# Optimization experiments

Measured on AMD Instinct MI355X. Metric: run time of the kernel, lower is better.

Reference implementation:

```python
import jax, jax.numpy as jnp
import numpy as np

EMBED_DIM = 256
NUM_HEADS = 8
PROJ_DIM = EMBED_DIM // NUM_HEADS


def setup_inputs() -> dict:
    key = jax.random.key(0)
    ks = jax.random.split(key, 5)
    scale = 1.0 / np.sqrt(EMBED_DIM)
    inputs = jax.random.normal(ks[0], (2, 12, 12, 12, EMBED_DIM), dtype=jnp.float32)
    Wq = jax.random.normal(ks[1], (EMBED_DIM, EMBED_DIM), dtype=jnp.float32) * scale
    Wk = jax.random.normal(ks[2], (EMBED_DIM, EMBED_DIM), dtype=jnp.float32) * scale
    Wv = jax.random.normal(ks[3], (EMBED_DIM, EMBED_DIM), dtype=jnp.float32) * scale
    Wo = jax.random.normal(ks[4], (EMBED_DIM, EMBED_DIM), dtype=jnp.float32) * scale
    z = jnp.zeros((EMBED_DIM,), dtype=jnp.float32)
    return {"inputs": inputs, "Wq": Wq, "bq": z, "Wk": Wk, "bk": z,
            "Wv": Wv, "bv": z, "Wo": Wo, "bo": z}


def reference(inputs, Wq, bq, Wk, bk, Wv, bv, Wo, bo):
    B, h, w, d, E = inputs.shape
    S = h * w * d  # flattened spatial sequence
    x = inputs.reshape(B, S, E)
    # projections + head split: [B, S, E] -> [B, H, S, P]
    def split_heads(t):
        return t.reshape(B, S, NUM_HEADS, PROJ_DIM).transpose(0, 2, 1, 3)
    q = split_heads(x @ Wq + bq)
    k = split_heads(x @ Wk + bk)
    v = split_heads(x @ Wv + bv)
    # NOTE: original module does NOT scale by 1/sqrt(proj_dim)
    scores = jnp.einsum('bhsp,bhtp->bhst', q, k)  # [B, H, S, S]
    attn = jax.nn.softmax(scores, axis=-1)
    out = jnp.einsum('bhst,bhtp->bhsp', attn, v)  # [B, H, S, P]
    out = out.transpose(0, 2, 1, 3).reshape(B, h, w, d, E)
    return out @ Wo + bo
```

## Files before the change

### kernel.cpp

```cpp
#include <hip/hip_runtime.h>
#include <math.h>

#define EMBED 256
#define HEADS 8
#define PDIM  32
#define BATCH 2
#define SEQ   1728
#define NTOK  (BATCH*SEQ)
#define NE    (NTOK*EMBED)
#define NKT   (SEQ/64)
#define NPAIR ((NKT+1)/2)
#define WSZ   (EMBED*EMBED)
#define XCH   (NE/8)
#define WCH   (WSZ/8)
#define LOG2E 1.44269504088896f

typedef __attribute__((ext_vector_type(8))) __bf16 bf16x8;
typedef __attribute__((ext_vector_type(4))) float  f32x4;
typedef unsigned short ushort_t;
typedef unsigned int   uint_t;

static __device__ __forceinline__ unsigned short f2bf_rne(float f) {
    union { float f; unsigned u; } x; x.f = f;
    unsigned r = x.u + 0x7fffu + ((x.u >> 16) & 1u);
    return (unsigned short)(r >> 16);
}
union v8cast { uint4 u; bf16x8 v; };

static __device__ __forceinline__ void cvt8_hilo(const float f[8], bf16x8& hi, bf16x8& lo) {
    uint4 ph, pl;
    uint_t* phv = (uint_t*)&ph; uint_t* plv = (uint_t*)&pl;
    #pragma unroll
    for (int j = 0; j < 4; ++j) {
        const float f0 = f[2 * j], f1 = f[2 * j + 1];
        const uint_t u0 = __float_as_uint(f0) + 0x8000u;
        const uint_t u1 = __float_as_uint(f1) + 0x8000u;
        phv[j] = __builtin_amdgcn_perm(u1, u0, 0x07060302u);
        const float l0 = f0 - __uint_as_float(u0 & 0xFFFF0000u);
        const float l1 = f1 - __uint_as_float(u1 & 0xFFFF0000u);
        plv[j] = __builtin_amdgcn_perm(__float_as_uint(l1) + 0x8000u,
                                       __float_as_uint(l0) + 0x8000u, 0x07060302u);
    }
    v8cast ch; ch.u = ph; hi = ch.v;
    v8cast cl; cl.u = pl; lo = cl.v;
}

__global__ __launch_bounds__(256) void prep_kernel(
    const float* __restrict__ x,
    const float* __restrict__ Wq, const float* __restrict__ Wk,
    const float* __restrict__ Wv, const float* __restrict__ Wo,
    ushort_t* __restrict__ xhi, ushort_t* __restrict__ xlo,
    ushort_t* __restrict__ wthi, ushort_t* __restrict__ wtlo,
    ushort_t* __restrict__ wot)
{
    const int id = blockIdx.x * 256 + threadIdx.x;
    if (id < XCH) {
        float f[8];
        *(float4*)&f[0] = *(const float4*)(x + (size_t)id * 8);
        *(float4*)&f[4] = *(const float4*)(x + (size_t)id * 8 + 4);
        bf16x8 hi, lo; cvt8_hilo(f, hi, lo);
        v8cast ch; ch.v = hi; *(uint4*)&xhi[(size_t)id * 8] = ch.u;
        v8cast cl; cl.v = lo; *(uint4*)&xlo[(size_t)id * 8] = cl.u;
    } else if (id < XCH + 3 * WCH) {
        int r = id - XCH;
        const int z = r / WCH; r -= z * WCH;
        const float* __restrict__ W = (z == 0) ? Wq : (z == 1) ? Wk : Wv;
        const int n = r >> 5, kc = (r & 31) * 8;
        float f[8];
        #pragma unroll
        for (int j = 0; j < 8; ++j) f[j] = W[(size_t)(kc + j) * EMBED + n];
        bf16x8 hi, lo; cvt8_hilo(f, hi, lo);
        v8cast ch; ch.v = hi; *(uint4*)&wthi[(size_t)z * WSZ + n * EMBED + kc] = ch.u;
        v8cast cl; cl.v = lo; *(uint4*)&wtlo[(size_t)z * WSZ + n * EMBED + kc] = cl.u;
    } else {
        int r = id - XCH - 3 * WCH;
        const int n = r >> 5, kc = (r & 31) * 8;
        float f[8];
        #pragma unroll
        for (int j = 0; j < 8; ++j) f[j] = Wo[(size_t)(kc + j) * EMBED + n];
        bf16x8 hi, lo; cvt8_hilo(f, hi, lo);
        v8cast ch; ch.v = hi; *(uint4*)&wot[n * EMBED + kc] = ch.u;
    }
}

__global__ __launch_bounds__(64) void qkv_gemm_kernel(
    const ushort_t* __restrict__ xhi, const ushort_t* __restrict__ xlo,
    const ushort_t* __restrict__ wthi, const ushort_t* __restrict__ wtlo,
    const float* __restrict__ bq, const float* __restrict__ bk, const float* __restrict__ bv,
    ushort_t* __restrict__ qo, ushort_t* __restrict__ ko, ushort_t* __restrict__ vt)
{
    const int lane = threadIdx.x, li = lane & 15, quad = lane >> 4;
    const int m0 = blockIdx.x * 32, n0 = blockIdx.y * 32, z = blockIdx.z;
    const float* __restrict__ bias = (z == 0) ? bq : (z == 1) ? bk : bv;

    const ushort_t* ahp = xhi + (size_t)(m0 + li) * EMBED + quad * 8;
    const ushort_t* alp = xlo + (size_t)(m0 + li) * EMBED + quad * 8;
    const ushort_t* bhp = wthi + (size_t)z * WSZ + (size_t)(n0 + li) * EMBED + quad * 8;
    const ushort_t* blp = wtlo + (size_t)z * WSZ + (size_t)(n0 + li) * EMBED + quad * 8;

    f32x4 acc[2][2];
    #pragma unroll
    for (int mt = 0; mt < 2; ++mt)
        #pragma unroll
        for (int nt = 0; nt < 2; ++nt)
            acc[mt][nt] = (f32x4){0.f, 0.f, 0.f, 0.f};

    #pragma unroll 2
    for (int k0 = 0; k0 < EMBED; k0 += 32) {
        bf16x8 ah[2], al[2], bh[2], bl[2];
        #pragma unroll
        for (int mt = 0; mt < 2; ++mt) {
            ah[mt] = *(const bf16x8*)(ahp + (size_t)mt * 16 * EMBED + k0);
            al[mt] = *(const bf16x8*)(alp + (size_t)mt * 16 * EMBED + k0);
        }
        #pragma unroll
        for (int nt = 0; nt < 2; ++nt) {
            bh[nt] = *(const bf16x8*)(bhp + (size_t)nt * 16 * EMBED + k0);
            bl[nt] = *(const bf16x8*)(blp + (size_t)nt * 16 * EMBED + k0);
        }
        #pragma unroll
        for (int mt = 0; mt < 2; ++mt)
            #pragma unroll
            for (int nt = 0; nt < 2; ++nt) {
                acc[mt][nt] = __builtin_amdgcn_mfma_f32_16x16x32_bf16(ah[mt], bh[nt], acc[mt][nt], 0, 0, 0);
                acc[mt][nt] = __builtin_amdgcn_mfma_f32_16x16x32_bf16(al[mt], bh[nt], acc[mt][nt], 0, 0, 0);
                acc[mt][nt] = __builtin_amdgcn_mfma_f32_16x16x32_bf16(ah[mt], bl[nt], acc[mt][nt], 0, 0, 0);
            }
    }

    const int b = m0 / SEQ;
    const int sbase = m0 - b * SEQ;

    if (z <= 1) {
        ushort_t* __restrict__ dst = z ? ko : qo;
        #pragma unroll
        for (int nt = 0; nt < 2; ++nt) {
            const int gcol = n0 + nt * 16 + li;
            const int h = gcol >> 5, p = gcol & 31;
            const float bb = bias[gcol];
            ushort_t* base = dst + ((size_t)(b * HEADS + h) * SEQ) * PDIM + p;
            #pragma unroll
            for (int mt = 0; mt < 2; ++mt)
                #pragma unroll
                for (int r = 0; r < 4; ++r) {
                    const int s = sbase + mt * 16 + quad * 4 + r;
                    base[(size_t)s * PDIM] = f2bf_rne(acc[mt][nt][r] + bb);
                }
        }
    } else {
        #pragma unroll
        for (int nt = 0; nt < 2; ++nt) {
            const int gcol = n0 + nt * 16 + li;
            const int h = gcol >> 5, p = gcol & 31;
            const float bb = bias[gcol];
            ushort_t* base = vt + ((size_t)(b * HEADS + h) * PDIM + p) * SEQ;
            #pragma unroll
            for (int mt = 0; mt < 2; ++mt) {
                const int s0 = sbase + mt * 16 + quad * 4;
                ushort4 w;
                w.x = f2bf_rne(acc[mt][nt][0] + bb);
                w.y = f2bf_rne(acc[mt][nt][1] + bb);
                w.z = f2bf_rne(acc[mt][nt][2] + bb);
                w.w = f2bf_rne(acc[mt][nt][3] + bb);
                *(ushort4*)&base[s0] = w;
            }
        }
    }
}

__global__ __launch_bounds__(512, 4) void attn_kernel(
    const ushort_t* __restrict__ q, const ushort_t* __restrict__ k,
    const ushort_t* __restrict__ vt, ushort_t* __restrict__ aob)
{
    const int t    = threadIdx.x;
    const int lane = t & 63;
    const int w    = t >> 6;
    const int li   = lane & 15;
    const int quad = lane >> 4;
    const int qg   = w >> 1, half = w & 1;
    const int bh = blockIdx.y;
    const int b  = bh >> 3, h = bh & 7;
    const int q0 = blockIdx.x * 64 + qg * 16;

    const ushort_t* __restrict__ qb = q  + (size_t)bh * SEQ * PDIM;
    const ushort_t* __restrict__ kb = k  + (size_t)bh * SEQ * PDIM;
    const ushort_t* __restrict__ vb = vt + (size_t)bh * PDIM * SEQ;

    __shared__ ushort_t Ks[2][2][64][40];
    __shared__ ushort_t Vs[2][2][32][72];
    __shared__ ushort_t Ps[8][16][72];
    __shared__ float    Om[8][16][33];
    __shared__ float    Ml[8][2][16];

    const bf16x8 qfrag = *(const bf16x8*)(qb + (size_t)(q0 + li) * PDIM + quad * 8);

    const int ktil = t >> 8;
    const int krow = (t >> 2) & 63, kck = (t & 3) * 8;
    const int vrow = (t >> 3) & 31, vcv = (t & 7) * 8;
    const ushort_t* kgp = kb + (size_t)(ktil * 64 + krow) * PDIM + kck;
    const ushort_t* vgp = vb + (size_t)vrow * SEQ + ktil * 64 + vcv;

    f32x4 o0 = {0.f, 0.f, 0.f, 0.f};
    f32x4 o1 = {0.f, 0.f, 0.f, 0.f};
    float m_run = -__builtin_inff(), l_run = 0.f;

    uint4 kreg = *(const uint4*)(kgp);
    uint4 vreg = *(const uint4*)(vgp);

    #pragma unroll 2
    for (int i = 0; i < NPAIR; ++i) {
        const int p = i & 1;
        *(uint4*)&Ks[p][ktil][krow][kck] = kreg;
        *(uint4*)&Vs[p][ktil][vrow][vcv] = vreg;
        __syncthreads();
        if (i + 1 < NPAIR && 2 * (i + 1) + ktil < NKT) {
            kreg = *(const uint4*)(kgp + (size_t)(2 * (i + 1)) * 64 * PDIM);
            vreg = *(const uint4*)(vgp + 2 * (i + 1) * 64);
        }
        const int kt = 2 * i + half;
        if (kt < NKT) {
            const f32x4 zero = {0.f, 0.f, 0.f, 0.f};
            f32x4 st[4];
            #pragma unroll
            for (int jt = 0; jt < 4; ++jt) {
                const bf16x8 kf = *(const bf16x8*)&Ks[p][half][jt * 16 + li][quad * 8];
                st[jt] = __builtin_amdgcn_mfma_f32_16x16x32_bf16(kf, qfrag, zero, 0, 0, 0);
            }

            float tm = fmaxf(fmaxf(fmaxf(st[0][0], st[0][1]), fmaxf(st[0][2], st[0][3])),
                             fmaxf(fmaxf(st[1][0], st[1][1]), fmaxf(st[1][2], st[1][3])));
            tm = fmaxf(tm, fmaxf(fmaxf(fmaxf(st[2][0], st[2][1]), fmaxf(st[2][2], st[2][3])),
                                 fmaxf(fmaxf(st[3][0], st[3][1]), fmaxf(st[3][2], st[3][3]))));
            tm = fmaxf(tm, __shfl_xor(tm, 16));
            tm = fmaxf(tm, __shfl_xor(tm, 32));
            const float mnew  = fmaxf(m_run, tm);
            const float negml = -(mnew * LOG2E);

            float ps = 0.f;
            #pragma unroll
            for (int jt = 0; jt < 4; ++jt) {
                const float p0 = __builtin_amdgcn_exp2f(fmaf(st[jt][0], LOG2E, negml));
                const float p1 = __builtin_amdgcn_exp2f(fmaf(st[jt][1], LOG2E, negml));
                const float p2 = __builtin_amdgcn_exp2f(fmaf(st[jt][2], LOG2E, negml));
                const float p3 = __builtin_amdgcn_exp2f(fmaf(st[jt][3], LOG2E, negml));
                ps += (p0 + p1) + (p2 + p3);
                uint2 pw;
                pw.x = __builtin_amdgcn_perm(__float_as_uint(p1) + 0x8000u,
                                             __float_as_uint(p0) + 0x8000u, 0x07060302u);
                pw.y = __builtin_amdgcn_perm(__float_as_uint(p3) + 0x8000u,
                                             __float_as_uint(p2) + 0x8000u, 0x07060302u);
                *(uint2*)&Ps[w][li][16 * jt + 4 * quad] = pw;
            }
            ps += __shfl_xor(ps, 16);
            ps += __shfl_xor(ps, 32);

            const float alpha = __builtin_amdgcn_exp2f(fmaf(m_run, LOG2E, negml));
            l_run = fmaf(l_run, alpha, ps);
            m_run = mnew;

            float af[4];
            #pragma unroll
            for (int r = 0; r < 4; ++r) af[r] = __shfl(alpha, 4 * quad + r);
            #pragma unroll
            for (int r = 0; r < 4; ++r) { o0[r] *= af[r]; o1[r] *= af[r]; }

            const bf16x8 pa0 = *(const bf16x8*)&Ps[w][li][8 * quad];
            const bf16x8 pa1 = *(const bf16x8*)&Ps[w][li][32 + 8 * quad];
            const bf16x8 vf00 = *(const bf16x8*)&Vs[p][half][li][quad * 8];
            const bf16x8 vf01 = *(const bf16x8*)&Vs[p][half][16 + li][quad * 8];
            const bf16x8 vf10 = *(const bf16x8*)&Vs[p][half][li][32 + quad * 8];
            const bf16x8 vf11 = *(const bf16x8*)&Vs[p][half][16 + li][32 + quad * 8];
            o0 = __builtin_amdgcn_mfma_f32_16x16x32_bf16(pa0, vf00, o0, 0, 0, 0);
            o0 = __builtin_amdgcn_mfma_f32_16x16x32_bf16(pa1, vf10, o0, 0, 0, 0);
            o1 = __builtin_amdgcn_mfma_f32_16x16x32_bf16(pa0, vf01, o1, 0, 0, 0);
            o1 = __builtin_amdgcn_mfma_f32_16x16x32_bf16(pa1, vf11, o1, 0, 0, 0);
        }
    }

    #pragma unroll
    for (int r = 0; r < 4; ++r) {
        Om[w][4 * quad + r][li]      = o0[r];
        Om[w][4 * quad + r][16 + li] = o1[r];
    }
    if (quad == 0) { Ml[w][0][li] = m_run; Ml[w][1][li] = l_run; }
    __syncthreads();

    const int wa = qg * 2, wb = wa + 1;
    const float ma = Ml[wa][0][li], mb = Ml[wb][0][li];
    const float mC = fmaxf(ma, mb);
    const float sa = __builtin_amdgcn_exp2f((ma - mC) * LOG2E);
    const float sb = __builtin_amdgcn_exp2f((mb - mC) * LOG2E);
    const float lC = Ml[wa][1][li] * sa + Ml[wb][1][li] * sb;
    const float inv = 1.0f / lC;
    const float fa = sa * inv, fb = sb * inv;
    const int c = half * 16 + li;
    #pragma unroll
    for (int r = 0; r < 4; ++r) {
        const int qq = 4 * quad + r;
        const float aq = __shfl(fa, qq);
        const float bq_ = __shfl(fb, qq);
        const float val = Om[wa][qq][c] * aq + Om[wb][qq][c] * bq_;
        const int s = q0 + qq;
        aob[((size_t)(b * SEQ + s)) * EMBED + h * PDIM + c] = f2bf_rne(val);
    }
}

__global__ __launch_bounds__(64) void out_gemm_kernel(
    const ushort_t* __restrict__ a, const ushort_t* __restrict__ wot,
    const float* __restrict__ bo, float* __restrict__ out)
{
    const int lane = threadIdx.x, li = lane & 15, quad = lane >> 4;
    const int m0 = blockIdx.x * 32, n0 = blockIdx.y * 16;

    const ushort_t* ap = a + (size_t)(m0 + li) * EMBED + quad * 8;
    const ushort_t* bp = wot + (size_t)(n0 + li) * EMBED + quad * 8;

    f32x4 acc[2];
    #pragma unroll
    for (int mt = 0; mt < 2; ++mt) acc[mt] = (f32x4){0.f, 0.f, 0.f, 0.f};

    #pragma unroll 2
    for (int k0 = 0; k0 < EMBED; k0 += 32) {
        bf16x8 ah[2];
        #pragma unroll
        for (int mt = 0; mt < 2; ++mt)
            ah[mt] = *(const bf16x8*)(ap + (size_t)mt * 16 * EMBED + k0);
        const bf16x8 bf = *(const bf16x8*)(bp + k0);
        #pragma unroll
        for (int mt = 0; mt < 2; ++mt)
            acc[mt] = __builtin_amdgcn_mfma_f32_16x16x32_bf16(ah[mt], bf, acc[mt], 0, 0, 0);
    }

    const float bb = bo[n0 + li];
    #pragma unroll
    for (int mt = 0; mt < 2; ++mt)
        #pragma unroll
        for (int r = 0; r < 4; ++r) {
            const int row = m0 + mt * 16 + quad * 4 + r;
            out[(size_t)row * EMBED + n0 + li] = acc[mt][r] + bb;
        }
}

extern "C" void kernel_launch(void* const* d_in, const int* in_sizes, int n_in,
                              void* d_out, int out_size, void* d_ws, size_t ws_size,
                              hipStream_t stream)
{
    const float* x  = (const float*)d_in[0];
    const float* Wq = (const float*)d_in[1];
    const float* bq = (const float*)d_in[2];
    const float* Wk = (const float*)d_in[3];
    const float* bk = (const float*)d_in[4];
    const float* Wv = (const float*)d_in[5];
    const float* bv = (const float*)d_in[6];
    const float* Wo = (const float*)d_in[7];
    const float* bo = (const float*)d_in[8];
    float* out = (float*)d_out;

    ushort_t* ws   = (ushort_t*)d_ws;
    ushort_t* qb   = ws;
    ushort_t* kb   = qb   + (size_t)NE;
    ushort_t* vtb  = kb   + (size_t)NE;
    ushort_t* aob  = vtb  + (size_t)NE;
    ushort_t* xhi  = aob  + (size_t)NE;
    ushort_t* xlo  = xhi  + (size_t)NE;
    ushort_t* wthi = xlo  + (size_t)NE;
    ushort_t* wtlo = wthi + (size_t)(3 * WSZ);
    ushort_t* wot  = wtlo + (size_t)(3 * WSZ);

    prep_kernel<<<dim3((XCH + 4 * WCH) / 256), 256, 0, stream>>>(
        x, Wq, Wk, Wv, Wo, xhi, xlo, wthi, wtlo, wot);
    qkv_gemm_kernel<<<dim3(NTOK / 32, 8, 3), 64, 0, stream>>>(
        xhi, xlo, wthi, wtlo, bq, bk, bv, qb, kb, vtb);
    attn_kernel<<<dim3(SEQ / 64, BATCH * HEADS), 512, 0, stream>>>(qb, kb, vtb, aob);
    out_gemm_kernel<<<dim3(NTOK / 32, 16), 64, 0, stream>>>(aob, wot, bo, out);
}
```

Baseline: 127.7 us.

## Fuse all stages into one persistent cooperative kernel with grid syncs

Replaces the four separate launches with a single cooperative persistent kernel of 432 blocks of 256 threads, using grid-wide syncs between prep, QKV GEMM, attention and output GEMM. Each stage becomes a grid-stride or per-wave work loop. The attention stage is restructured from 8 waves that split the key range in halves and merge partial results through LDS to 4 waves that each own 16 queries over all key tiles, which removes the Om/Ml merge step. The aim is to cut launch gaps and inter-kernel overhead. In exchange each stage is limited to a fixed grid of 432 blocks, the grid syncs add cost, and attention loses the key-split parallelism, so per-wave work grows. Separate kernels remain as a fallback if the cooperative launch fails.

```diff
diff --git a/kernel.cpp b/kernel.cpp
--- a/kernel.cpp
+++ b/kernel.cpp
@@ -1,5 +1,8 @@
 #include <hip/hip_runtime.h>
+#include <hip/hip_cooperative_groups.h>
 #include <math.h>
+
+namespace cg = cooperative_groups;
 
 #define EMBED 256
 #define HEADS 8
@@ -9,10 +12,14 @@
 #define NTOK  (BATCH*SEQ)
 #define NE    (NTOK*EMBED)
 #define NKT   (SEQ/64)
-#define NPAIR ((NKT+1)/2)
 #define WSZ   (EMBED*EMBED)
 #define XCH   (NE/8)
 #define WCH   (WSZ/8)
+#define NBLK  432
+#define NTHR  256
+#define TOTTHR  (NBLK*NTHR)
+#define TOTWAVE (TOTTHR/64)
+#define QKV_UNITS 2592
 #define LOG2E 1.44269504088896f
 
 typedef __attribute__((ext_vector_type(8))) __bf16 bf16x8;
@@ -45,7 +52,13 @@
     v8cast cl; cl.u = pl; lo = cl.v;
 }
 
-__global__ __launch_bounds__(256) void prep_kernel(
+struct AttnLds {
+    ushort_t Ks[2][64][40];
+    ushort_t Vs[2][32][72];
+    ushort_t Ps[4][16][72];
+};
+
+static __device__ __forceinline__ void dev_prep(
     const float* __restrict__ x,
     const float* __restrict__ Wq, const float* __restrict__ Wk,
     const float* __restrict__ Wv, const float* __restrict__ Wo,
@@ -53,122 +66,132 @@
     ushort_t* __restrict__ wthi, ushort_t* __restrict__ wtlo,
     ushort_t* __restrict__ wot)
 {
-    const int id = blockIdx.x * 256 + threadIdx.x;
-    if (id < XCH) {
-        float f[8];
-        *(float4*)&f[0] = *(const float4*)(x + (size_t)id * 8);
-        *(float4*)&f[4] = *(const float4*)(x + (size_t)id * 8 + 4);
-        bf16x8 hi, lo; cvt8_hilo(f, hi, lo);
-        v8cast ch; ch.v = hi; *(uint4*)&xhi[(size_t)id * 8] = ch.u;
-        v8cast cl; cl.v = lo; *(uint4*)&xlo[(size_t)id * 8] = cl.u;
-    } else if (id < XCH + 3 * WCH) {
-        int r = id - XCH;
-        const int z = r / WCH; r -= z * WCH;
-        const float* __restrict__ W = (z == 0) ? Wq : (z == 1) ? Wk : Wv;
-        const int n = r >> 5, kc = (r & 31) * 8;
-        float f[8];
-        #pragma unroll
-        for (int j = 0; j < 8; ++j) f[j] = W[(size_t)(kc + j) * EMBED + n];
-        bf16x8 hi, lo; cvt8_hilo(f, hi, lo);
-        v8cast ch; ch.v = hi; *(uint4*)&wthi[(size_t)z * WSZ + n * EMBED + kc] = ch.u;
-        v8cast cl; cl.v = lo; *(uint4*)&wtlo[(size_t)z * WSZ + n * EMBED + kc] = cl.u;
-    } else {
-        int r = id - XCH - 3 * WCH;
-        const int n = r >> 5, kc = (r & 31) * 8;
-        float f[8];
-        #pragma unroll
-        for (int j = 0; j < 8; ++j) f[j] = Wo[(size_t)(kc + j) * EMBED + n];
-        bf16x8 hi, lo; cvt8_hilo(f, hi, lo);
-        v8cast ch; ch.v = hi; *(uint4*)&wot[n * EMBED + kc] = ch.u;
-    }
-}
-
-__global__ __launch_bounds__(64) void qkv_gemm_kernel(
+    const int tid = blockIdx.x * NTHR + threadIdx.x;
+    for (int id = tid; id < XCH + 4 * WCH; id += TOTTHR) {
+        if (id < XCH) {
+            float f[8];
+            *(float4*)&f[0] = *(const float4*)(x + (size_t)id * 8);
+            *(float4*)&f[4] = *(const float4*)(x + (size_t)id * 8 + 4);
+            bf16x8 hi, lo; cvt8_hilo(f, hi, lo);
+            v8cast ch; ch.v = hi; *(uint4*)&xhi[(size_t)id * 8] = ch.u;
+            v8cast cl; cl.v = lo; *(uint4*)&xlo[(size_t)id * 8] = cl.u;
+        } else if (id < XCH + 3 * WCH) {
+            int r = id - XCH;
+            const int z = r >> 13; r &= (WCH - 1);
+            const float* __restrict__ W = (z == 0) ? Wq : (z == 1) ? Wk : Wv;
+            const int n = r >> 5, kc = (r & 31) * 8;
+            float f[8];
+            #pragma unroll
+            for (int j = 0; j < 8; ++j) f[j] = W[(size_t)(kc + j) * EMBED + n];
+            bf16x8 hi, lo; cvt8_hilo(f, hi, lo);
+            v8cast ch; ch.v = hi; *(uint4*)&wthi[(size_t)z * WSZ + n * EMBED + kc] = ch.u;
+            v8cast cl; cl.v = lo; *(uint4*)&wtlo[(size_t)z * WSZ + n * EMBED + kc] = cl.u;
+        } else {
+            int r = id - XCH - 3 * WCH;
+            const int n = r >> 5, kc = (r & 31) * 8;
+            float f[8];
+            #pragma unroll
+            for (int j = 0; j < 8; ++j) f[j] = Wo[(size_t)(kc + j) * EMBED + n];
+            bf16x8 hi, lo; cvt8_hilo(f, hi, lo);
+            v8cast ch; ch.v = hi; *(uint4*)&wot[n * EMBED + kc] = ch.u;
+        }
+    }
+}
+
+static __device__ __forceinline__ void dev_qkv(
     const ushort_t* __restrict__ xhi, const ushort_t* __restrict__ xlo,
     const ushort_t* __restrict__ wthi, const ushort_t* __restrict__ wtlo,
     const float* __restrict__ bq, const float* __restrict__ bk, const float* __restrict__ bv,
     ushort_t* __restrict__ qo, ushort_t* __restrict__ ko, ushort_t* __restrict__ vt)
 {
-    const int lane = threadIdx.x, li = lane & 15, quad = lane >> 4;
-    const int m0 = blockIdx.x * 32, n0 = blockIdx.y * 32, z = blockIdx.z;
-    const float* __restrict__ bias = (z == 0) ? bq : (z == 1) ? bk : bv;
-
-    const ushort_t* ahp = xhi + (size_t)(m0 + li) * EMBED + quad * 8;
-    const ushort_t* alp = xlo + (size_t)(m0 + li) * EMBED + quad * 8;
-    const ushort_t* bhp = wthi + (size_t)z * WSZ + (size_t)(n0 + li) * EMBED + quad * 8;
-    const ushort_t* blp = wtlo + (size_t)z * WSZ + (size_t)(n0 + li) * EMBED + quad * 8;
-
-    f32x4 acc[2][2];
-    #pragma unroll
-    for (int mt = 0; mt < 2; ++mt)
-        #pragma unroll
-        for (int nt = 0; nt < 2; ++nt)
-            acc[mt][nt] = (f32x4){0.f, 0.f, 0.f, 0.f};
-
-    #pragma unroll 2
-    for (int k0 = 0; k0 < EMBED; k0 += 32) {
-        bf16x8 ah[2], al[2], bh[2], bl[2];
-        #pragma unroll
-        for (int mt = 0; mt < 2; ++mt) {
-            ah[mt] = *(const bf16x8*)(ahp + (size_t)mt * 16 * EMBED + k0);
-            al[mt] = *(const bf16x8*)(alp + (size_t)mt * 16 * EMBED + k0);
-        }
-        #pragma unroll
-        for (int nt = 0; nt < 2; ++nt) {
-            bh[nt] = *(const bf16x8*)(bhp + (size_t)nt * 16 * EMBED + k0);
-            bl[nt] = *(const bf16x8*)(blp + (size_t)nt * 16 * EMBED + k0);
-        }
+    const int lane = threadIdx.x & 63, li = lane & 15, quad = lane >> 4;
+    const int gw = blockIdx.x * (NTHR / 64) + (threadIdx.x >> 6);
+    for (int u = gw; u < QKV_UNITS; u += TOTWAVE) {
+        const int z   = u / 864;
+        const int rem = u - z * 864;
+        const int nb  = rem / 108;
+        const int mb  = rem - nb * 108;
+        const int m0 = mb * 32, n0 = nb * 32;
+        const float* __restrict__ bias = (z == 0) ? bq : (z == 1) ? bk : bv;
+
+        const ushort_t* ahp = xhi + (size_t)(m0 + li) * EMBED + quad * 8;
+        const ushort_t* alp = xlo + (size_t)(m0 + li) * EMBED + quad * 8;
+        const ushort_t* bhp = wthi + (size_t)z * WSZ + (size_t)(n0 + li) * EMBED + quad * 8;
+        const ushort_t* blp = wtlo + (size_t)z * WSZ + (size_t)(n0 + li) * EMBED + quad * 8;
+
+        f32x4 acc[2][2];
         #pragma unroll
         for (int mt = 0; mt < 2; ++mt)
             #pragma unroll
+            for (int nt = 0; nt < 2; ++nt)
+                acc[mt][nt] = (f32x4){0.f, 0.f, 0.f, 0.f};
+
+        #pragma unroll 2
+        for (int k0 = 0; k0 < EMBED; k0 += 32) {
+            bf16x8 ah[2], al[2], bh[2], bl[2];
+            #pragma unroll
+            for (int mt = 0; mt < 2; ++mt) {
+                ah[mt] = *(const bf16x8*)(ahp + (size_t)mt * 16 * EMBED + k0);
+                al[mt] = *(const bf16x8*)(alp + (size_t)mt * 16 * EMBED + k0);
+            }
+            #pragma unroll
             for (int nt = 0; nt < 2; ++nt) {
-                acc[mt][nt] = __builtin_amdgcn_mfma_f32_16x16x32_bf16(ah[mt], bh[nt], acc[mt][nt], 0, 0, 0);
-                acc[mt][nt] = __builtin_amdgcn_mfma_f32_16x16x32_bf16(al[mt], bh[nt], acc[mt][nt], 0, 0, 0);
-                acc[mt][nt] = __builtin_amdgcn_mfma_f32_16x16x32_bf16(ah[mt], bl[nt], acc[mt][nt], 0, 0, 0);
+                bh[nt] = *(const bf16x8*)(bhp + (size_t)nt * 16 * EMBED + k0);
+                bl[nt] = *(const bf16x8*)(blp + (size_t)nt * 16 * EMBED + k0);
             }
-    }
-
-    const int b = m0 / SEQ;
-    const int sbase = m0 - b * SEQ;
-
-    if (z <= 1) {
-        ushort_t* __restrict__ dst = z ? ko : qo;
-        #pragma unroll
-        for (int nt = 0; nt < 2; ++nt) {
-            const int gcol = n0 + nt * 16 + li;
-            const int h = gcol >> 5, p = gcol & 31;
-            const float bb = bias[gcol];
-            ushort_t* base = dst + ((size_t)(b * HEADS + h) * SEQ) * PDIM + p;
             #pragma unroll
             for (int mt = 0; mt < 2; ++mt)
                 #pragma unroll
-                for (int r = 0; r < 4; ++r) {
-                    const int s = sbase + mt * 16 + quad * 4 + r;
-                    base[(size_t)s * PDIM] = f2bf_rne(acc[mt][nt][r] + bb);
+                for (int nt = 0; nt < 2; ++nt) {
+                    acc[mt][nt] = __builtin_amdgcn_mfma_f32_16x16x32_bf16(ah[mt], bh[nt], acc[mt][nt], 0, 0, 0);
+                    acc[mt][nt] = __builtin_amdgcn_mfma_f32_16x16x32_bf16(al[mt], bh[nt], acc[mt][nt], 0, 0, 0);
+                    acc[mt][nt] = __builtin_amdgcn_mfma_f32_16x16x32_bf16(ah[mt], bl[nt], acc[mt][nt], 0, 0, 0);
                 }
         }
-    } else {
-        #pragma unroll
-        for (int nt = 0; nt < 2; ++nt) {
-            const int gcol = n0 + nt * 16 + li;
-            const int h = gcol >> 5, p = gcol & 31;
-            const float bb = bias[gcol];
-            ushort_t* base = vt + ((size_t)(b * HEADS + h) * PDIM + p) * SEQ;
-            #pragma unroll
-            for (int mt = 0; mt < 2; ++mt) {
-                const int s0 = sbase + mt * 16 + quad * 4;
-                ushort4 w;
-                w.x = f2bf_rne(acc[mt][nt][0] + bb);
-                w.y = f2bf_rne(acc[mt][nt][1] + bb);
-                w.z = f2bf_rne(acc[mt][nt][2] + bb);
-                w.w = f2bf_rne(acc[mt][nt][3] + bb);
-                *(ushort4*)&base[s0] = w;
+
+        const int b = m0 / SEQ;
+        const int sbase = m0 - b * SEQ;
+
+        if (z <= 1) {
+            ushort_t* __restrict__ dst = z ? ko : qo;
+            #pragma unroll
+            for (int nt = 0; nt < 2; ++nt) {
+                const int gcol = n0 + nt * 16 + li;
+                const int h = gcol >> 5, p = gcol & 31;
+                const float bb = bias[gcol];
+                ushort_t* base = dst + ((size_t)(b * HEADS + h) * SEQ) * PDIM + p;
+                #pragma unroll
+                for (int mt = 0; mt < 2; ++mt)
+                    #pragma unroll
+                    for (int r = 0; r < 4; ++r) {
+                        const int s = sbase + mt * 16 + quad * 4 + r;
+                        base[(size_t)s * PDIM] = f2bf_rne(acc[mt][nt][r] + bb);
+                    }
             }
-        }
-    }
-}
-
-__global__ __launch_bounds__(512, 4) void attn_kernel(
+        } else {
+            #pragma unroll
+            for (int nt = 0; nt < 2; ++nt) {
+                const int gcol = n0 + nt * 16 + li;
+                const int h = gcol >> 5, p = gcol & 31;
+                const float bb = bias[gcol];
+                ushort_t* base = vt + ((size_t)(b * HEADS + h) * PDIM + p) * SEQ;
+                #pragma unroll
+                for (int mt = 0; mt < 2; ++mt) {
+                    const int s0 = sbase + mt * 16 + quad * 4;
+                    ushort4 w;
+                    w.x = f2bf_rne(acc[mt][nt][0] + bb);
+                    w.y = f2bf_rne(acc[mt][nt][1] + bb);
+                    w.z = f2bf_rne(acc[mt][nt][2] + bb);
+                    w.w = f2bf_rne(acc[mt][nt][3] + bb);
+                    *(ushort4*)&base[s0] = w;
+                }
+            }
+        }
+    }
+}
+
+static __device__ __forceinline__ void dev_attn(
+    AttnLds& S,
     const ushort_t* __restrict__ q, const ushort_t* __restrict__ k,
     const ushort_t* __restrict__ vt, ushort_t* __restrict__ aob)
 {
@@ -177,28 +200,22 @@
     const int w    = t >> 6;
     const int li   = lane & 15;
     const int quad = lane >> 4;
-    const int qg   = w >> 1, half = w & 1;
-    const int bh = blockIdx.y;
+    const int bid  = blockIdx.x;
+    const int qt   = bid % 27;
+    const int bh   = bid / 27;
     const int b  = bh >> 3, h = bh & 7;
-    const int q0 = blockIdx.x * 64 + qg * 16;
+    const int q0 = qt * 64 + w * 16;
 
     const ushort_t* __restrict__ qb = q  + (size_t)bh * SEQ * PDIM;
     const ushort_t* __restrict__ kb = k  + (size_t)bh * SEQ * PDIM;
     const ushort_t* __restrict__ vb = vt + (size_t)bh * PDIM * SEQ;
 
-    __shared__ ushort_t Ks[2][2][64][40];
-    __shared__ ushort_t Vs[2][2][32][72];
-    __shared__ ushort_t Ps[8][16][72];
-    __shared__ float    Om[8][16][33];
-    __shared__ float    Ml[8][2][16];
-
     const bf16x8 qfrag = *(const bf16x8*)(qb + (size_t)(q0 + li) * PDIM + quad * 8);
 
-    const int ktil = t >> 8;
-    const int krow = (t >> 2) & 63, kck = (t & 3) * 8;
-    const int vrow = (t >> 3) & 31, vcv = (t & 7) * 8;
-    const ushort_t* kgp = kb + (size_t)(ktil * 64 + krow) * PDIM + kck;
-    const ushort_t* vgp = vb + (size_t)vrow * SEQ + ktil * 64 + vcv;
+    const int jk = w * 16 + (lane >> 2), ck = (lane & 3) * 8;
+    const int pv = w * 8 + (lane >> 3),  cv = (lane & 7) * 8;
+    const ushort_t* kgp = kb + (size_t)jk * PDIM + ck;
+    const ushort_t* vgp = vb + (size_t)pv * SEQ + cv;
 
     f32x4 o0 = {0.f, 0.f, 0.f, 0.f};
     f32x4 o1 = {0.f, 0.f, 0.f, 0.f};
@@ -207,110 +224,94 @@
     uint4 kreg = *(const uint4*)(kgp);
     uint4 vreg = *(const uint4*)(vgp);
 
-    #pragma unroll 2
-    for (int i = 0; i < NPAIR; ++i) {
-        const int p = i & 1;
-        *(uint4*)&Ks[p][ktil][krow][kck] = kreg;
-        *(uint4*)&Vs[p][ktil][vrow][vcv] = vreg;
+    for (int kt = 0; kt < NKT; ++kt) {
+        const int p = kt & 1;
+        *(uint4*)&S.Ks[p][jk][ck] = kreg;
+        *(uint4*)&S.Vs[p][pv][cv] = vreg;
         __syncthreads();
-        if (i + 1 < NPAIR && 2 * (i + 1) + ktil < NKT) {
-            kreg = *(const uint4*)(kgp + (size_t)(2 * (i + 1)) * 64 * PDIM);
-            vreg = *(const uint4*)(vgp + 2 * (i + 1) * 64);
-        }
-        const int kt = 2 * i + half;
-        if (kt < NKT) {
-            const f32x4 zero = {0.f, 0.f, 0.f, 0.f};
-            f32x4 st[4];
-            #pragma unroll
-            for (int jt = 0; jt < 4; ++jt) {
-                const bf16x8 kf = *(const bf16x8*)&Ks[p][half][jt * 16 + li][quad * 8];
-                st[jt] = __builtin_amdgcn_mfma_f32_16x16x32_bf16(kf, qfrag, zero, 0, 0, 0);
-            }
-
-            float tm = fmaxf(fmaxf(fmaxf(st[0][0], st[0][1]), fmaxf(st[0][2], st[0][3])),
-                             fmaxf(fmaxf(st[1][0], st[1][1]), fmaxf(st[1][2], st[1][3])));
-            tm = fmaxf(tm, fmaxf(fmaxf(fmaxf(st[2][0], st[2][1]), fmaxf(st[2][2], st[2][3])),
-                                 fmaxf(fmaxf(st[3][0], st[3][1]), fmaxf(st[3][2], st[3][3]))));
-            tm = fmaxf(tm, __shfl_xor(tm, 16));
-            tm = fmaxf(tm, __shfl_xor(tm, 32));
-            const float mnew  = fmaxf(m_run, tm);
-            const float negml = -(mnew * LOG2E);
-
-            float ps = 0.f;
-            #pragma unroll
-            for (int jt = 0; jt < 4; ++jt) {
-                const float p0 = __builtin_amdgcn_exp2f(fmaf(st[jt][0], LOG2E, negml));
-                const float p1 = __builtin_amdgcn_exp2f(fmaf(st[jt][1], LOG2E, negml));
-                const float p2 = __builtin_amdgcn_exp2f(fmaf(st[jt][2], LOG2E, negml));
-                const float p3 = __builtin_amdgcn_exp2f(fmaf(st[jt][3], LOG2E, negml));
-                ps += (p0 + p1) + (p2 + p3);
-                uint2 pw;
-                pw.x = __builtin_amdgcn_perm(__float_as_uint(p1) + 0x8000u,
-                                             __float_as_uint(p0) + 0x8000u, 0x07060302u);
-                pw.y = __builtin_amdgcn_perm(__float_as_uint(p3) + 0x8000u,
-                                             __float_as_uint(p2) + 0x8000u, 0x07060302u);
-                *(uint2*)&Ps[w][li][16 * jt + 4 * quad] = pw;
-            }
-            ps += __shfl_xor(ps, 16);
-            ps += __shfl_xor(ps, 32);
-
-            const float alpha = __builtin_amdgcn_exp2f(fmaf(m_run, LOG2E, negml));
-            l_run = fmaf(l_run, alpha, ps);
-            m_run = mnew;
-
-            float af[4];
-            #pragma unroll
-            for (int r = 0; r < 4; ++r) af[r] = __shfl(alpha, 4 * quad + r);
-            #pragma unroll
-            for (int r = 0; r < 4; ++r) { o0[r] *= af[r]; o1[r] *= af[r]; }
-
-            const bf16x8 pa0 = *(const bf16x8*)&Ps[w][li][8 * quad];
-            const bf16x8 pa1 = *(const bf16x8*)&Ps[w][li][32 + 8 * quad];
-            const bf16x8 vf00 = *(const bf16x8*)&Vs[p][half][li][quad * 8];
-            const bf16x8 vf01 = *(const bf16x8*)&Vs[p][half][16 + li][quad * 8];
-            const bf16x8 vf10 = *(const bf16x8*)&Vs[p][half][li][32 + quad * 8];
-            const bf16x8 vf11 = *(const bf16x8*)&Vs[p][half][16 + li][32 + quad * 8];
-            o0 = __builtin_amdgcn_mfma_f32_16x16x32_bf16(pa0, vf00, o0, 0, 0, 0);
-            o0 = __builtin_amdgcn_mfma_f32_16x16x32_bf16(pa1, vf10, o0, 0, 0, 0);
-            o1 = __builtin_amdgcn_mfma_f32_16x16x32_bf16(pa0, vf01, o1, 0, 0, 0);
-            o1 = __builtin_amdgcn_mfma_f32_16x16x32_bf16(pa1, vf11, o1, 0, 0, 0);
-        }
-    }
-
+        if (kt + 1 < NKT) {
+            kreg = *(const uint4*)(kgp + (size_t)(kt + 1) * 64 * PDIM);
+            vreg = *(const uint4*)(vgp + (kt + 1) * 64);
+        }
+
+        const f32x4 zero = {0.f, 0.f, 0.f, 0.f};
+        f32x4 st[4];
+        #pragma unroll
+        for (int jt = 0; jt < 4; ++jt) {
+            const bf16x8 kf = *(const bf16x8*)&S.Ks[p][jt * 16 + li][quad * 8];
+            st[jt] = __builtin_amdgcn_mfma_f32_16x16x32_bf16(kf, qfrag, zero, 0, 0, 0);
+        }
+
+        float tm = st[0][0];
+        #pragma unroll
+        for (int jt = 0; jt < 4; ++jt)
+            #pragma unroll
+            for (int r = 0; r < 4; ++r) tm = fmaxf(tm, st[jt][r]);
+        tm = fmaxf(tm, __shfl_xor(tm, 16));
+        tm = fmaxf(tm, __shfl_xor(tm, 32));
+        const float mnew  = fmaxf(m_run, tm);
+        const float negml = -(mnew * LOG2E);
+
+        float ps = 0.f;
+        #pragma unroll
+        for (int jt = 0; jt < 4; ++jt) {
+            const float p0 = __builtin_amdgcn_exp2f(fmaf(st[jt][0], LOG2E, negml));
+            const float p1 = __builtin_amdgcn_exp2f(fmaf(st[jt][1], LOG2E, negml));
+            const float p2 = __builtin_amdgcn_exp2f(fmaf(st[jt][2], LOG2E, negml));
+            const float p3 = __builtin_amdgcn_exp2f(fmaf(st[jt][3], LOG2E, negml));
+            ps += (p0 + p1) + (p2 + p3);
+            uint2 pw;
+            pw.x = __builtin_amdgcn_perm(__float_as_uint(p1) + 0x8000u,
+                                         __float_as_uint(p0) + 0x8000u, 0x07060302u);
+            pw.y = __builtin_amdgcn_perm(__float_as_uint(p3) + 0x8000u,
+                                         __float_as_uint(p2) + 0x8000u, 0x07060302u);
+            *(uint2*)&S.Ps[w][li][16 * jt + 4 * quad] = pw;
+        }
+        ps += __shfl_xor(ps, 16);
+        ps += __shfl_xor(ps, 32);
+
+        const float alpha = __builtin_amdgcn_exp2f(fmaf(m_run, LOG2E, negml));
+        l_run = fmaf(l_run, alpha, ps);
+        m_run = mnew;
+
+        float af[4];
+        #pragma unroll
+        for (int r = 0; r < 4; ++r) af[r] = __shfl(alpha, 4 * quad + r);
+        #pragma unroll
+        for (int r = 0; r < 4; ++r) { o0[r] *= af[r]; o1[r] *= af[r]; }
+
+        const bf16x8 pa0 = *(const bf16x8*)&S.Ps[w][li][8 * quad];
+        const bf16x8 pa1 = *(const bf16x8*)&S.Ps[w][li][32 + 8 * quad];
+        const bf16x8 vf00 = *(const bf16x8*)&S.Vs[p][li][quad * 8];
+        const bf16x8 vf01 = *(const bf16x8*)&S.Vs[p][16 + li][quad * 8];
+        const bf16x8 vf10 = *(const bf16x8*)&S.Vs[p][li][32 + quad * 8];
+        const bf16x8 vf11 = *(const bf16x8*)&S.Vs[p][16 + li][32 + quad * 8];
+        o0 = __builtin_amdgcn_mfma_f32_16x16x32_bf16(pa0, vf00, o0, 0, 0, 0);
+        o0 = __builtin_amdgcn_mfma_f32_16x16x32_bf16(pa1, vf10, o0, 0, 0, 0);
+        o1 = __builtin_amdgcn_mfma_f32_16x16x32_bf16(pa0, vf01, o1, 0, 0, 0);
+        o1 = __builtin_amdgcn_mfma_f32_16x16x32_bf16(pa1, vf11, o1, 0, 0, 0);
+    }
+
+    float linv[4];
+    #pragma unroll
+    for (int r = 0; r < 4; ++r) linv[r] = 1.0f / __shfl(l_run, 4 * quad + r);
     #pragma unroll
     for (int r = 0; r < 4; ++r) {
-        Om[w][4 * quad + r][li]      = o0[r];
-        Om[w][4 * quad + r][16 + li] = o1[r];
-    }
-    if (quad == 0) { Ml[w][0][li] = m_run; Ml[w][1][li] = l_run; }
-    __syncthreads();
-
-    const int wa = qg * 2, wb = wa + 1;
-    const float ma = Ml[wa][0][li], mb = Ml[wb][0][li];
-    const float mC = fmaxf(ma, mb);
-    const float sa = __builtin_amdgcn_exp2f((ma - mC) * LOG2E);
-    const float sb = __builtin_amdgcn_exp2f((mb - mC) * LOG2E);
-    const float lC = Ml[wa][1][li] * sa + Ml[wb][1][li] * sb;
-    const float inv = 1.0f / lC;
-    const float fa = sa * inv, fb = sb * inv;
-    const int c = half * 16 + li;
-    #pragma unroll
-    for (int r = 0; r < 4; ++r) {
-        const int qq = 4 * quad + r;
-        const float aq = __shfl(fa, qq);
-        const float bq_ = __shfl(fb, qq);
-        const float val = Om[wa][qq][c] * aq + Om[wb][qq][c] * bq_;
-        const int s = q0 + qq;
-        aob[((size_t)(b * SEQ + s)) * EMBED + h * PDIM + c] = f2bf_rne(val);
-    }
-}
-
-__global__ __launch_bounds__(64) void out_gemm_kernel(
+        const int s = q0 + 4 * quad + r;
+        ushort_t* row = aob + ((size_t)(b * SEQ + s)) * EMBED + h * PDIM;
+        row[li]      = f2bf_rne(o0[r] * linv[r]);
+        row[16 + li] = f2bf_rne(o1[r] * linv[r]);
+    }
+}
+
+static __device__ __forceinline__ void dev_out(
     const ushort_t* __restrict__ a, const ushort_t* __restrict__ wot,
     const float* __restrict__ bo, float* __restrict__ out)
 {
-    const int lane = threadIdx.x, li = lane & 15, quad = lane >> 4;
-    const int m0 = blockIdx.x * 32, n0 = blockIdx.y * 16;
+    const int lane = threadIdx.x & 63, li = lane & 15, quad = lane >> 4;
+    const int gw = blockIdx.x * (NTHR / 64) + (threadIdx.x >> 6);
+    const int nb = gw / 108, mb = gw - nb * 108;
+    const int m0 = mb * 32, n0 = nb * 16;
 
     const ushort_t* ap = a + (size_t)(m0 + li) * EMBED + quad * 8;
     const ushort_t* bp = wot + (size_t)(n0 + li) * EMBED + quad * 8;
@@ -340,6 +341,55 @@
             out[(size_t)row * EMBED + n0 + li] = acc[mt][r] + bb;
         }
 }
+
+__global__ __launch_bounds__(256, 2) void fused_kernel(
+    const float* __restrict__ x,
+    const float* __restrict__ Wq, const float* __restrict__ bq,
+    const float* __restrict__ Wk, const float* __restrict__ bk,
+    const float* __restrict__ Wv, const float* __restrict__ bv,
+    const float* __restrict__ Wo, const float* __restrict__ bo,
+    float* __restrict__ out,
+    ushort_t* __restrict__ qb, ushort_t* __restrict__ kb,
+    ushort_t* __restrict__ vtb, ushort_t* __restrict__ aob,
+    ushort_t* __restrict__ xhi, ushort_t* __restrict__ xlo,
+    ushort_t* __restrict__ wthi, ushort_t* __restrict__ wtlo,
+    ushort_t* __restrict__ wot)
+{
+    __shared__ AttnLds S;
+    dev_prep(x, Wq, Wk, Wv, Wo, xhi, xlo, wthi, wtlo, wot);
+    cg::this_grid().sync();
+    dev_qkv(xhi, xlo, wthi, wtlo, bq, bk, bv, qb, kb, vtb);
+    cg::this_grid().sync();
+    dev_attn(S, qb, kb, vtb, aob);
+    cg::this_grid().sync();
+    dev_out(aob, wot, bo, out);
+}
+
+__global__ __launch_bounds__(256, 2) void prep_k(
+    const float* __restrict__ x, const float* __restrict__ Wq,
+    const float* __restrict__ Wk, const float* __restrict__ Wv,
+    const float* __restrict__ Wo, ushort_t* __restrict__ xhi,
+    ushort_t* __restrict__ xlo, ushort_t* __restrict__ wthi,
+    ushort_t* __restrict__ wtlo, ushort_t* __restrict__ wot)
+{ dev_prep(x, Wq, Wk, Wv, Wo, xhi, xlo, wthi, wtlo, wot); }
+
+__global__ __launch_bounds__(256, 2) void qkv_k(
+    const ushort_t* __restrict__ xhi, const ushort_t* __restrict__ xlo,
+    const ushort_t* __restrict__ wthi, const ushort_t* __restrict__ wtlo,
+    const float* __restrict__ bq, const float* __restrict__ bk,
+    const float* __restrict__ bv, ushort_t* __restrict__ qo,
+    ushort_t* __restrict__ ko, ushort_t* __restrict__ vt)
+{ dev_qkv(xhi, xlo, wthi, wtlo, bq, bk, bv, qo, ko, vt); }
+
+__global__ __launch_bounds__(256, 2) void attn_k(
+    const ushort_t* __restrict__ q, const ushort_t* __restrict__ k,
+    const ushort_t* __restrict__ vt, ushort_t* __restrict__ aob)
+{ __shared__ AttnLds S; dev_attn(S, q, k, vt, aob); }
+
+__global__ __launch_bounds__(256, 2) void out_k(
+    const ushort_t* __restrict__ a, const ushort_t* __restrict__ wot,
+    const float* __restrict__ bo, float* __restrict__ out)
+{ dev_out(a, wot, bo, out); }
 
 extern "C" void kernel_launch(void* const* d_in, const int* in_sizes, int n_in,
                               void* d_out, int out_size, void* d_ws, size_t ws_size,
@@ -367,10 +417,24 @@
     ushort_t* wtlo = wthi + (size_t)(3 * WSZ);
     ushort_t* wot  = wtlo + (size_t)(3 * WSZ);
 
-    prep_kernel<<<dim3((XCH + 4 * WCH) / 256), 256, 0, stream>>>(
-        x, Wq, Wk, Wv, Wo, xhi, xlo, wthi, wtlo, wot);
-    qkv_gemm_kernel<<<dim3(NTOK / 32, 8, 3), 64, 0, stream>>>(
-        xhi, xlo, wthi, wtlo, bq, bk, bv, qb, kb, vtb);
-    attn_kernel<<<dim3(SEQ / 64, BATCH * HEADS), 512, 0, stream>>>(qb, kb, vtb, aob);
-    out_gemm_kernel<<<dim3(NTOK / 32, 16), 64, 0, stream>>>(aob, wot, bo, out);
-}
+    void* args[] = {
+        (void*)&x, (void*)&Wq, (void*)&bq, (void*)&Wk, (void*)&bk,
+        (void*)&Wv, (void*)&bv, (void*)&Wo, (void*)&bo, (void*)&out,
+        (void*)&qb, (void*)&kb, (void*)&vtb, (void*)&aob,
+        (void*)&xhi, (void*)&xlo, (void*)&wthi, (void*)&wtlo, (void*)&wot
+    };
+
+    hipError_t err = hipLaunchCooperativeKernel(
+        reinterpret_cast<void*>(fused_kernel),
+        dim3(NBLK), dim3(NTHR), args, 0, stream);
+
+    if (err != hipSuccess) {
+        (void)hipGetLastError();
+        prep_k<<<dim3(NBLK), dim3(NTHR), 0, stream>>>(
+            x, Wq, Wk, Wv, Wo, xhi, xlo, wthi, wtlo, wot);
+        qkv_k<<<dim3(NBLK), dim3(NTHR), 0, stream>>>(
+            xhi, xlo, wthi, wtlo, bq, bk, bv, qb, kb, vtb);
+        attn_k<<<dim3(NBLK), dim3(NTHR), 0, stream>>>(qb, kb, vtb, aob);
+        out_k<<<dim3(NBLK), dim3(NTHR), 0, stream>>>(aob, wot, bo, out);
+    }
+}
```

Measured after the change: 301.2 us. +135.8%, slower.
